# Kernel optimization log

Hardware: AMD Instinct MI355X
Metric: run time of the kernel (lower is better)

## Reference

```python
import jax, jax.numpy as jnp
import numpy as np

SIZE = 7  # grid size; H = W = SIZE


def setup_inputs() -> dict:
    key = jax.random.key(0)
    k1, k2, k3, k4 = jax.random.split(key, 4)
    N, C = 256, 2048
    x = jax.random.normal(k1, (N, C, SIZE, SIZE), dtype=jnp.float32)
    mask = jax.random.uniform(k2, (N, SIZE, SIZE), dtype=jnp.float32)
    W = jax.random.normal(k3, (2, 2 * C), dtype=jnp.float32) * 0.02
    b = jax.random.normal(k4, (2,), dtype=jnp.float32) * 0.02
    return {"x": x, "mask": mask, "W": W, "b": b}


def reference(x, mask, W, b):
    N, C, H, Wd = x.shape
    HW = H * Wd
    size = float(H)
    # (N, HW, C) tokens
    reduced_x = jnp.transpose(x.reshape(N, C, HW), (0, 2, 1))
    m = mask.reshape(N, HW)
    thr = jnp.mean(m, axis=1, keepdims=True)  # curr_coef = 1.0
    binary_mask = (m > thr).astype(x.dtype)  # (N, HW)
    # mean over channels of masked tokens, then argmax over positions
    masked_mean = jnp.mean(reduced_x * binary_mask[:, :, None], axis=-1)  # (N, HW)
    max_index = jnp.argmax(masked_mean, axis=-1)  # (N,)
    batch_idx = jnp.arange(N)
    max_features = reduced_x[batch_idx, max_index]  # (N, C)
    # concat(max_feature, token) -> tiny linear 2C -> 2 with ReLU
    disc = jnp.concatenate(
        [jnp.broadcast_to(max_features[:, None, :], (N, HW, C)), reduced_x], axis=-1
    )  # (N, HW, 2C)
    preds_coord = jax.nn.relu(jnp.einsum('npc,oc->npo', disc, W) + b)  # (N, HW, 2)
    # zero out prediction at the anchor position
    preds_coord = preds_coord.at[batch_idx, max_index].set(0.0)
    # polar-coordinate targets relative to anchor
    ii, jj = jnp.meshgrid(jnp.arange(H), jnp.arange(Wd), indexing='ij')
    label = jnp.stack([ii, jj], axis=-1).astype(x.dtype).reshape(HW, 2)  # (HW, 2)
    basic_anchor = label[max_index][:, None, :]  # (N, 1, 2)
    rel = (label[None, :, :] - basic_anchor) / size  # (N, HW, 2)
    relative_dist = jnp.sqrt(jnp.sum(rel ** 2, axis=-1))  # (N, HW)
    relative_angle = jnp.arctan2(rel[:, :, 1], rel[:, :, 0])
    relative_angle = (relative_angle / jnp.float32(np.pi) + 1.0) / 2.0  # (N, HW)
    preds_dist = preds_coord[:, :, 0]
    preds_angle = preds_coord[:, :, 1]
    dist_loss = (preds_dist - relative_dist) ** 2
    gap = preds_angle - relative_angle
    gap = jnp.where(gap < 0, gap + 1.0, gap)
    gap = gap - jnp.mean(gap, axis=-1, keepdims=True)
    angle_loss = gap ** 2
    return (dist_loss + angle_loss).reshape(N, H, Wd)
```

## Files before the change

### kernel.cpp

```cpp
#include <hip/hip_runtime.h>
#include <math.h>

#define N_     256
#define C_     2048
#define HW_    49
#define CHUNKS 4
#define CPB    (C_/CHUNKS)
#define TILE_C 64
#define NTILE  (CPB/TILE_C)
#define NG     5
#define TILE_BYTES (TILE_C*HW_*4)

__device__ __forceinline__ void cp16(const void* gptr, unsigned lds_off) {
  __builtin_amdgcn_global_load_lds(
      (const __attribute__((address_space(1))) unsigned int*)gptr,
      (__attribute__((address_space(3))) unsigned int*)lds_off,
      16, 0, 0);
}

__device__ __forceinline__ void stage_tile(const float* src, unsigned lb,
                                           int wave, int lane) {
  const char* s = (const char*)src;
  #pragma unroll
  for (int i = 0; i < 3; ++i) {
    const int seg = wave + i*4;
    cp16(s + seg*1024 + lane*16, lb + (unsigned)(seg*1024));
  }
  if (lane < 4)
    cp16(s + 12288 + wave*64 + lane*16, lb + (unsigned)(12288 + wave*64));
}

__global__ __launch_bounds__(256) void k_reduce(const float* __restrict__ x,
                                                const float* __restrict__ Wm,
                                                float* __restrict__ part) {
  const int chunk = blockIdx.x;
  const int n     = blockIdx.y;
  const int t     = threadIdx.x;
  const int wave  = t >> 6;
  const int lane  = t & 63;

  __shared__ __align__(16) float  buf[2][TILE_C*HW_];
  __shared__ float4 wt4[CPB];

  const unsigned lb0 = (unsigned)(size_t)&buf[0][0];
  const unsigned lb1 = (unsigned)(size_t)&buf[1][0];

  const float* xbase = x + ((size_t)n*C_ + (size_t)chunk*CPB)*HW_;

  for (int c = t; c < CPB; c += 256) {
    const int gc = chunk*CPB + c;
    float4 w;
    w.x = Wm[0*(2*C_)       + gc];
    w.y = Wm[1*(2*C_)       + gc];
    w.z = Wm[0*(2*C_) + C_  + gc];
    w.w = Wm[1*(2*C_) + C_  + gc];
    wt4[c] = w;
  }

  stage_tile(xbase, lb0, wave, lane);

  asm volatile("s_waitcnt lgkmcnt(0)" ::: "memory");
  __builtin_amdgcn_s_barrier();

  const int  p   = lane;
  const bool act = (wave == 0) && (lane < HW_);

  float a0 = 0.f, a1 = 0.f, a2 = 0.f, a3 = 0.f, a4 = 0.f;

  for (int tt = 0; tt < NTILE; ++tt) {
    if (tt < NTILE-1) {
      stage_tile(xbase + (size_t)(tt+1)*TILE_C*HW_,
                 (tt & 1) ? lb0 : lb1, wave, lane);
      asm volatile("s_waitcnt vmcnt(4)" ::: "memory");
    } else {
      asm volatile("s_waitcnt vmcnt(0)" ::: "memory");
    }
    __builtin_amdgcn_s_barrier();

    if (act) {
      const float*  tl = buf[tt & 1];
      const float4* wp = &wt4[tt*TILE_C];
      #pragma unroll 16
      for (int c = 0; c < TILE_C; ++c) {
        const float  v = tl[c*HW_ + p];
        const float4 w = wp[c];
        a0 += v;
        a1 = fmaf(v, w.x, a1);
        a2 = fmaf(v, w.y, a2);
        a3 = fmaf(v, w.z, a3);
        a4 = fmaf(v, w.w, a4);
      }
    }
    asm volatile("s_waitcnt lgkmcnt(0)" ::: "memory");
    __builtin_amdgcn_s_barrier();
  }

  if (act) {
    float* dst = part + ((size_t)n*CHUNKS + chunk)*(NG*HW_);
    dst[0*HW_ + p] = a0;
    dst[1*HW_ + p] = a1;
    dst[2*HW_ + p] = a2;
    dst[3*HW_ + p] = a3;
    dst[4*HW_ + p] = a4;
  }
}

__global__ __launch_bounds__(256) void k_final(const float* __restrict__ part,
                                               const float* __restrict__ mask,
                                               const float* __restrict__ b,
                                               float* __restrict__ out) {
  const int n = blockIdx.x;
  const int t = threadIdx.x;
  __shared__ float red[NG*HW_];

  if (t < NG*HW_) {
    float a = 0.f;
    #pragma unroll
    for (int ch = 0; ch < CHUNKS; ++ch)
      a += part[((size_t)n*CHUNKS + ch)*(NG*HW_) + t];
    red[t] = a;
  }
  __syncthreads();

  if (t < 64) {
    const int  p   = t;
    const bool act = (p < HW_);

    float m = act ? mask[n*HW_ + p] : 0.f;
    float tot = m;
    #pragma unroll
    for (int off = 32; off; off >>= 1) tot += __shfl_xor(tot, off);
    const float thr = tot / 49.f;

    float s  = act ? red[0*HW_ + p] : 0.f;
    float mm = act ? ((m > thr) ? (s * (1.f/2048.f)) : 0.f) : -INFINITY;
    float best = mm;
    int   bidx = act ? p : 64;
    #pragma unroll
    for (int off = 32; off; off >>= 1) {
      float ov = __shfl_xor(best, off);
      int   oi = __shfl_xor(bidx, off);
      if (ov > best || (ov == best && oi < bidx)) { best = ov; bidx = oi; }
    }
    const int mi = bidx;

    const float u0mi = red[1*HW_ + mi];
    const float u1mi = red[2*HW_ + mi];

    float pred0 = 0.f, pred1 = 0.f;
    if (act) {
      pred0 = fmaxf(u0mi + red[3*HW_ + p] + b[0], 0.f);
      pred1 = fmaxf(u1mi + red[4*HW_ + p] + b[1], 0.f);
      if (p == mi) { pred0 = 0.f; pred1 = 0.f; }
    }

    const int ii = p / 7,  jj = p - ii*7;
    const int ai = mi / 7, aj = mi - ai*7;
    const float ri = (float)(ii - ai) / 7.f;
    const float rj = (float)(jj - aj) / 7.f;
    const float dist = sqrtf(ri*ri + rj*rj);
    const float ang  = (atan2f(rj, ri) / 3.14159274101257324f + 1.f) * 0.5f;

    float gap = pred1 - ang;
    if (gap < 0.f) gap += 1.f;
    float gsum = act ? gap : 0.f;
    #pragma unroll
    for (int off = 32; off; off >>= 1) gsum += __shfl_xor(gsum, off);
    const float gmean = gsum / 49.f;

    if (act) {
      const float dl = pred0 - dist;
      const float ga = gap - gmean;
      out[n*HW_ + p] = dl*dl + ga*ga;
    }
  }
}

extern "C" void kernel_launch(void* const* d_in, const int* in_sizes, int n_in,
                              void* d_out, int out_size, void* d_ws, size_t ws_size,
                              hipStream_t stream) {
  const float* x    = (const float*)d_in[0];
  const float* mask = (const float*)d_in[1];
  const float* Wm   = (const float*)d_in[2];
  const float* b    = (const float*)d_in[3];
  float* out  = (float*)d_out;
  float* part = (float*)d_ws;

  dim3 g1(CHUNKS, N_);
  k_reduce<<<g1, 256, 0, stream>>>(x, Wm, part);
  k_final<<<N_, 256, 0, stream>>>(part, mask, b, out);
}
```

Baseline: 159.2 us.

## Give each wave its own channel slice with private double-buffered LDS staging

Instead of one wave computing while all four waves jointly stage tiles behind block barriers, each wave now streams its own quarter of the block's channels into a private double buffer and accumulates independently. The block-wide barriers in the loop go away and all four waves do arithmetic. Chunks per sample drop to two, so the final kernel now sums eight partials instead of four. Previously three of four waves sat idle during compute. The change also raises LDS use and adds more partial-sum traffic.

```diff
diff --git a/kernel.cpp b/kernel.cpp
--- a/kernel.cpp
+++ b/kernel.cpp
@@ -4,12 +4,14 @@
 #define N_     256
 #define C_     2048
 #define HW_    49
-#define CHUNKS 4
+#define CHUNKS 2
 #define CPB    (C_/CHUNKS)
-#define TILE_C 64
-#define NTILE  (CPB/TILE_C)
+#define WCH    (CPB/4)
+#define TILE_C 32
+#define NTILE  (WCH/TILE_C)
 #define NG     5
-#define TILE_BYTES (TILE_C*HW_*4)
+#define PARTS  (CHUNKS*4)
+#define TBYTES (TILE_C*HW_*4)
 
 __device__ __forceinline__ void cp16(const void* gptr, unsigned lds_off) {
   __builtin_amdgcn_global_load_lds(
@@ -19,15 +21,13 @@
 }
 
 __device__ __forceinline__ void stage_tile(const float* src, unsigned lb,
-                                           int wave, int lane) {
+                                           int lane) {
   const char* s = (const char*)src;
   #pragma unroll
-  for (int i = 0; i < 3; ++i) {
-    const int seg = wave + i*4;
-    cp16(s + seg*1024 + lane*16, lb + (unsigned)(seg*1024));
-  }
-  if (lane < 4)
-    cp16(s + 12288 + wave*64 + lane*16, lb + (unsigned)(12288 + wave*64));
+  for (int i = 0; i < 6; ++i)
+    cp16(s + i*1024 + lane*16, lb + (unsigned)(i*1024));
+  if (lane < 8)
+    cp16(s + 6144 + lane*16, lb + 6144u);
 }
 
 __global__ __launch_bounds__(256) void k_reduce(const float* __restrict__ x,
@@ -39,14 +39,10 @@
   const int wave  = t >> 6;
   const int lane  = t & 63;
 
-  __shared__ __align__(16) float  buf[2][TILE_C*HW_];
+  __shared__ __align__(16) float buf[4][2][TILE_C*HW_];
   __shared__ float4 wt4[CPB];
 
-  const unsigned lb0 = (unsigned)(size_t)&buf[0][0];
-  const unsigned lb1 = (unsigned)(size_t)&buf[1][0];
-
-  const float* xbase = x + ((size_t)n*C_ + (size_t)chunk*CPB)*HW_;
-
+  #pragma unroll
   for (int c = t; c < CPB; c += 256) {
     const int gc = chunk*CPB + c;
     float4 w;
@@ -56,31 +52,34 @@
     w.w = Wm[1*(2*C_) + C_  + gc];
     wt4[c] = w;
   }
+  __syncthreads();
 
-  stage_tile(xbase, lb0, wave, lane);
+  const float* wbase = x + ((size_t)n*C_ + (size_t)chunk*CPB
+                            + (size_t)wave*WCH)*HW_;
+  const unsigned lb0 = (unsigned)(size_t)&buf[wave][0][0];
+  const unsigned lb1 = (unsigned)(size_t)&buf[wave][1][0];
 
-  asm volatile("s_waitcnt lgkmcnt(0)" ::: "memory");
-  __builtin_amdgcn_s_barrier();
+  stage_tile(wbase, lb0, lane);
 
   const int  p   = lane;
-  const bool act = (wave == 0) && (lane < HW_);
+  const bool act = (lane < HW_);
 
   float a0 = 0.f, a1 = 0.f, a2 = 0.f, a3 = 0.f, a4 = 0.f;
 
+  #pragma unroll 2
   for (int tt = 0; tt < NTILE; ++tt) {
     if (tt < NTILE-1) {
-      stage_tile(xbase + (size_t)(tt+1)*TILE_C*HW_,
-                 (tt & 1) ? lb0 : lb1, wave, lane);
-      asm volatile("s_waitcnt vmcnt(4)" ::: "memory");
+      stage_tile(wbase + (size_t)(tt+1)*TILE_C*HW_,
+                 (tt & 1) ? lb0 : lb1, lane);
+      asm volatile("s_waitcnt vmcnt(7)" ::: "memory");
     } else {
       asm volatile("s_waitcnt vmcnt(0)" ::: "memory");
     }
-    __builtin_amdgcn_s_barrier();
 
     if (act) {
-      const float*  tl = buf[tt & 1];
-      const float4* wp = &wt4[tt*TILE_C];
-      #pragma unroll 16
+      const float*  tl = &buf[wave][tt & 1][0];
+      const float4* wp = &wt4[wave*WCH + tt*TILE_C];
+      #pragma unroll 8
       for (int c = 0; c < TILE_C; ++c) {
         const float  v = tl[c*HW_ + p];
         const float4 w = wp[c];
@@ -92,11 +91,10 @@
       }
     }
     asm volatile("s_waitcnt lgkmcnt(0)" ::: "memory");
-    __builtin_amdgcn_s_barrier();
   }
 
   if (act) {
-    float* dst = part + ((size_t)n*CHUNKS + chunk)*(NG*HW_);
+    float* dst = part + ((size_t)n*PARTS + (size_t)(chunk*4 + wave))*(NG*HW_);
     dst[0*HW_ + p] = a0;
     dst[1*HW_ + p] = a1;
     dst[2*HW_ + p] = a2;
@@ -116,8 +114,8 @@
   if (t < NG*HW_) {
     float a = 0.f;
     #pragma unroll
-    for (int ch = 0; ch < CHUNKS; ++ch)
-      a += part[((size_t)n*CHUNKS + ch)*(NG*HW_) + t];
+    for (int ch = 0; ch < PARTS; ++ch)
+      a += part[((size_t)n*PARTS + ch)*(NG*HW_) + t];
     red[t] = a;
   }
   __syncthreads();
```

Result: no change. 159.0 us (-0.1%).
